# Kernel tuning notes

Measured on AMD Instinct MI355X. Metric: run time of the kernel, lower is better.

The kernel has to match this reference:

```python
import jax, jax.numpy as jnp
import numpy as np

B, T, C, K, NC = 256, 240, 512, 64, 4  # batch, chunk_size, dim, clusters, num_classes+1
EPS = 1e-12


def setup_inputs() -> dict:
    key = jax.random.key(0)
    k1, k2, k3, k4 = jax.random.split(key, 4)
    inputs = jax.random.normal(k1, (B, T, C), dtype=jnp.float32)
    conv_w = jax.random.normal(k2, (K, C), dtype=jnp.float32) * 0.05   # 1x1 assignment conv, no bias (vladv2=False)
    centroids = jax.random.normal(k3, (K, C), dtype=jnp.float32)
    fc_w = jax.random.normal(k4, (NC, K * C), dtype=jnp.float32) * 0.02
    fc_b = jnp.zeros((NC,), dtype=jnp.float32)
    return {"inputs": inputs, "conv_w": conv_w, "centroids": centroids, "fc_w": fc_w, "fc_b": fc_b}


def _l2norm(x, axis):
    return x / jnp.clip(jnp.linalg.norm(x, axis=axis, keepdims=True), EPS)


def reference(inputs, conv_w, centroids, fc_w, fc_b):
    # inputs: [B, T, C]. Torch permutes to NCHW=(B, C, T, 1); feature dim = C.
    x = _l2norm(inputs, axis=-1)                      # normalize_input over feature dim
    # soft assignment: 1x1 conv -> logits [B, T, K], softmax over clusters
    a = jax.nn.softmax(jnp.einsum('btc,kc->btk', x, conv_w), axis=-1)
    # vlad[b,k,c] = sum_t a[b,t,k] * (x[b,t,c] - centroids[k,c])
    #            = einsum(a, x) - (sum_t a) * centroids   (avoids [B,K,C,T] intermediate)
    vlad = jnp.einsum('btk,btc->bkc', a, x) - a.sum(axis=1)[:, :, None] * centroids[None]
    vlad = _l2norm(vlad, axis=-1)                     # intra-normalization over C
    v = vlad.reshape(vlad.shape[0], -1)               # [B, K*C]
    v = _l2norm(v, axis=-1)                           # final L2 normalize
    # dropout is identity in eval mode; fc + sigmoid
    return jax.nn.sigmoid(v @ fc_w.T + fc_b)
```

## Files before the change

kernel.cpp:

```cpp
#include <hip/hip_runtime.h>
#include <hip/hip_bf16.h>
#include <stdint.h>

#define BB 256
#define TT 240
#define CC 512
#define KK 64
#define NCLS 4
#define CHUNK 32
#define NCHUNK 8
#define THREADS 512

typedef __attribute__((ext_vector_type(8))) short bf16x8;
typedef __attribute__((ext_vector_type(4))) float f32x4;

__device__ __forceinline__ unsigned short f2bf(float f) {
    union { float f; unsigned int i; } x; x.f = f;
    unsigned int r = x.i + 0x7FFFu + ((x.i >> 16) & 1u);
    return (unsigned short)(r >> 16);
}
__device__ __forceinline__ unsigned int pk2(float lo, float hi) {
    return ((unsigned int)f2bf(hi) << 16) | (unsigned int)f2bf(lo);
}
__device__ __forceinline__ void LB() {
    asm volatile("s_waitcnt lgkmcnt(0)\n\ts_barrier" ::: "memory");
}

struct alignas(16) SMemChunk {
    unsigned short x[CHUNK][520];
    unsigned short xT[CC][40];
    float logitsA[CHUNK][65];
    unsigned short aT[KK][40];
};
struct alignas(16) SMemEpi { unsigned short vbuf[KK * CC]; };
union SMemU { SMemChunk c; SMemEpi e; };

__global__ __launch_bounds__(THREADS, 2) void netvlad_kernel(
    const float* __restrict__ inp,
    const float* __restrict__ convw,
    const float* __restrict__ cent,
    const float* __restrict__ fcw,
    const float* __restrict__ fcb,
    float* __restrict__ out)
{
    __shared__ SMemU sm;
    __shared__ float sumsq_sh[CHUNK];
    __shared__ float asum[KK];
    __shared__ float ssred[2][KK];
    __shared__ float gred[8];
    __shared__ float fcred[8][NCLS];
    __shared__ float vinv_sh;

    const int tid  = threadIdx.x;
    const int b    = blockIdx.x;
    const int w    = tid >> 6;
    const int lane = tid & 63;
    const int grp  = (lane >> 4) & 3;
    const int col  = lane & 15;
    const int w2   = w >> 1;
    const int half = w & 1;

    if (tid < KK) asum[tid] = 0.f;

    f32x4 acc[16];
    #pragma unroll
    for (int j = 0; j < 16; ++j) acc[j] = (f32x4){0.f, 0.f, 0.f, 0.f};

    bf16x8 cw[16];
    #pragma unroll
    for (int ks = 0; ks < 16; ++ks) {
        const float* p = convw + (size_t)(w2 * 16 + col) * CC + ks * 32 + grp * 8;
        float4 a0 = *(const float4*)p;
        float4 a1 = *(const float4*)(p + 4);
        bf16x8 v;
        v[0] = (short)f2bf(a0.x); v[1] = (short)f2bf(a0.y);
        v[2] = (short)f2bf(a0.z); v[3] = (short)f2bf(a0.w);
        v[4] = (short)f2bf(a1.x); v[5] = (short)f2bf(a1.y);
        v[6] = (short)f2bf(a1.z); v[7] = (short)f2bf(a1.w);
        cw[ks] = v;
    }

    const size_t ibase = (size_t)b * (TT * CC);

    float4 r0[4], r1[4];
    #pragma unroll
    for (int i = 0; i < 4; ++i) {
        int g = tid + i * THREADS;
        int t = g >> 6, c8 = (g & 63) << 3;
        const float* p = inp + ibase + (size_t)t * CC + c8;
        r0[i] = *(const float4*)p;
        r1[i] = *(const float4*)(p + 4);
    }

    for (int ch = 0; ch < NCHUNK; ++ch) {
        const int t0 = ch * CHUNK;
        const int tvalid = (TT - t0 < CHUNK) ? (TT - t0) : CHUNK;

        #pragma unroll
        for (int i = 0; i < 4; ++i) {
            int g = tid + i * THREADS;
            int t = g >> 6, c8 = (g & 63) << 3;
            float4 u0 = r0[i], u1 = r1[i];
            uint4 val = (uint4){pk2(u0.x, u0.y), pk2(u0.z, u0.w),
                                pk2(u1.x, u1.y), pk2(u1.z, u1.w)};
            float s = u0.x*u0.x + u0.y*u0.y + u0.z*u0.z + u0.w*u0.w
                    + u1.x*u1.x + u1.y*u1.y + u1.z*u1.z + u1.w*u1.w;
            if (t >= tvalid) { val = (uint4){0u,0u,0u,0u}; s = 0.f; }
            *(uint4*)&sm.c.x[t][c8] = val;
            s += __shfl_xor(s, 1);  s += __shfl_xor(s, 2);  s += __shfl_xor(s, 4);
            s += __shfl_xor(s, 8);  s += __shfl_xor(s, 16); s += __shfl_xor(s, 32);
            if (lane == 0) sumsq_sh[t] = s;
        }
        if (ch + 1 < NCHUNK) {
            int nt0 = t0 + CHUNK;
            #pragma unroll
            for (int i = 0; i < 4; ++i) {
                int g = tid + i * THREADS;
                int t = g >> 6, c8 = (g & 63) << 3;
                int gt = nt0 + t; if (gt > TT - 1) gt = TT - 1;
                const float* p = inp + ibase + (size_t)gt * CC + c8;
                r0[i] = *(const float4*)p;
                r1[i] = *(const float4*)(p + 4);
            }
        }
        LB();

        {
            int c = tid;
            #pragma unroll
            for (int tb = 0; tb < 4; ++tb) {
                bf16x8 v;
                #pragma unroll
                for (int j = 0; j < 8; ++j) v[j] = (short)sm.c.x[tb * 8 + j][c];
                *(bf16x8*)&sm.c.xT[c][tb * 8] = v;
            }
        }

        {
            f32x4 lt = (f32x4){0.f, 0.f, 0.f, 0.f};
            #pragma unroll
            for (int ks = 0; ks < 16; ++ks) {
                bf16x8 bb = *(const bf16x8*)&sm.c.x[half * 16 + col][ks * 32 + grp * 8];
                lt = __builtin_amdgcn_mfma_f32_16x16x32_bf16(cw[ks], bb, lt, 0, 0, 0);
            }
            #pragma unroll
            for (int r = 0; r < 4; ++r)
                sm.c.logitsA[half * 16 + col][w2 * 16 + grp * 4 + r] = lt[r];
        }
        LB();

        {
            int t = tid >> 4, part = tid & 15;
            float rinv = 1.f / fmaxf(sqrtf(sumsq_sh[t]), 1e-12f);
            rinv = (t < tvalid) ? rinv : 0.f;

            float l[4]; float lmax = -1e30f;
            #pragma unroll
            for (int q = 0; q < 4; ++q) {
                l[q] = sm.c.logitsA[t][q * 16 + part] * rinv;
                lmax = fmaxf(lmax, l[q]);
            }
            lmax = fmaxf(lmax, __shfl_xor(lmax, 1));
            lmax = fmaxf(lmax, __shfl_xor(lmax, 2));
            lmax = fmaxf(lmax, __shfl_xor(lmax, 4));
            lmax = fmaxf(lmax, __shfl_xor(lmax, 8));
            float es = 0.f;
            #pragma unroll
            for (int q = 0; q < 4; ++q) { l[q] = __expf(l[q] - lmax); es += l[q]; }
            es += __shfl_xor(es, 1); es += __shfl_xor(es, 2);
            es += __shfl_xor(es, 4); es += __shfl_xor(es, 8);
            float is = 1.f / es;
            #pragma unroll
            for (int q = 0; q < 4; ++q) {
                float a = l[q] * is;
                sm.c.logitsA[t][q * 16 + part] = a;
                sm.c.aT[q * 16 + part][t] = (unsigned short)f2bf(a * rinv);
            }
        }
        LB();

        if (tid < KK) {
            float s = 0.f;
            for (int t = 0; t < tvalid; ++t) s += sm.c.logitsA[t][tid];
            asum[tid] += s;
        }

        {
            bf16x8 af = *(const bf16x8*)&sm.c.aT[w2 * 16 + col][grp * 8];
            #pragma unroll
            for (int j = 0; j < 16; ++j) {
                bf16x8 bf = *(const bf16x8*)&sm.c.xT[half * 256 + j * 16 + col][grp * 8];
                acc[j] = __builtin_amdgcn_mfma_f32_16x16x32_bf16(af, bf, acc[j], 0, 0, 0);
            }
        }
    }

    LB();

    #pragma unroll
    for (int r = 0; r < 4; ++r) {
        int cl = w2 * 16 + grp * 4 + r;
        float as = asum[cl];
        float ss = 0.f;
        #pragma unroll
        for (int j = 0; j < 16; ++j) {
            int c = half * 256 + j * 16 + col;
            float v = acc[j][r] - as * cent[(size_t)cl * CC + c];
            acc[j][r] = v;
            ss += v * v;
        }
        ss += __shfl_xor(ss, 1); ss += __shfl_xor(ss, 2);
        ss += __shfl_xor(ss, 4); ss += __shfl_xor(ss, 8);
        if (col == 0) ssred[half][cl] = ss;
    }
    LB();

    float contrib = 0.f;
    #pragma unroll
    for (int r = 0; r < 4; ++r) {
        int cl = w2 * 16 + grp * 4 + r;
        float ss = ssred[0][cl] + ssred[1][cl];
        float inv = 1.f / fmaxf(sqrtf(ss), 1e-12f);
        #pragma unroll
        for (int j = 0; j < 16; ++j) {
            float v = acc[j][r] * inv;
            acc[j][r] = v;
            contrib += v * v;
        }
    }
    #pragma unroll
    for (int m = 1; m < 64; m <<= 1) contrib += __shfl_xor(contrib, m);
    if (lane == 0) gred[w] = contrib;
    LB();
    if (tid == 0) {
        float tot = 0.f;
        #pragma unroll
        for (int i = 0; i < 8; ++i) tot += gred[i];
        vinv_sh = 1.f / fmaxf(sqrtf(tot), 1e-12f);
    }
    LB();

    {
        float vinv = vinv_sh;
        #pragma unroll
        for (int r = 0; r < 4; ++r) {
            int cl = w2 * 16 + grp * 4 + r;
            #pragma unroll
            for (int j = 0; j < 16; ++j) {
                int c = half * 256 + j * 16 + col;
                sm.e.vbuf[cl * CC + c] = f2bf(acc[j][r] * vinv);
            }
        }
    }
    LB();

    float pacc[NCLS] = {0.f, 0.f, 0.f, 0.f};
    #pragma unroll
    for (int i = 0; i < 8; ++i) {
        int idx = i * 4096 + tid * 8;
        bf16x8 vv = *(const bf16x8*)&sm.e.vbuf[idx];
        float vf[8];
        #pragma unroll
        for (int h = 0; h < 8; ++h) {
            union { unsigned int u; float f; } cvt;
            cvt.u = ((unsigned int)(unsigned short)vv[h]) << 16;
            vf[h] = cvt.f;
        }
        #pragma unroll
        for (int nc = 0; nc < NCLS; ++nc) {
            const float* wp = fcw + (size_t)nc * (KK * CC) + idx;
            float4 w0 = *(const float4*)wp;
            float4 w1 = *(const float4*)(wp + 4);
            pacc[nc] += vf[0] * w0.x + vf[1] * w0.y + vf[2] * w0.z + vf[3] * w0.w
                      + vf[4] * w1.x + vf[5] * w1.y + vf[6] * w1.z + vf[7] * w1.w;
        }
    }
    #pragma unroll
    for (int nc = 0; nc < NCLS; ++nc) {
        #pragma unroll
        for (int m = 1; m < 64; m <<= 1) pacc[nc] += __shfl_xor(pacc[nc], m);
    }
    if (lane == 0) {
        #pragma unroll
        for (int nc = 0; nc < NCLS; ++nc) fcred[w][nc] = pacc[nc];
    }
    LB();
    if (tid < NCLS) {
        float s = fcb[tid];
        #pragma unroll
        for (int ww = 0; ww < 8; ++ww) s += fcred[ww][tid];
        out[b * NCLS + tid] = 1.f / (1.f + __expf(-s));
    }
}

extern "C" void kernel_launch(void* const* d_in, const int* in_sizes, int n_in,
                              void* d_out, int out_size, void* d_ws, size_t ws_size,
                              hipStream_t stream) {
    const float* inp   = (const float*)d_in[0];
    const float* convw = (const float*)d_in[1];
    const float* cent  = (const float*)d_in[2];
    const float* fcw   = (const float*)d_in[3];
    const float* fcb   = (const float*)d_in[4];
    float* o = (float*)d_out;
    netvlad_kernel<<<BB, THREADS, 0, stream>>>(inp, convw, cent, fcw, fcb, o);
}
```

Measured before the change: 206.2 us.

## Double threads per block to 1024 and split logits GEMM over K halves

```diff
diff --git a/kernel.cpp b/kernel.cpp
--- a/kernel.cpp
+++ b/kernel.cpp
@@ -9,7 +9,7 @@
 #define NCLS 4
 #define CHUNK 32
 #define NCHUNK 8
-#define THREADS 512
+#define THREADS 1024
 
 typedef __attribute__((ext_vector_type(8))) short bf16x8;
 typedef __attribute__((ext_vector_type(4))) float f32x4;
@@ -19,8 +19,10 @@
     unsigned int r = x.i + 0x7FFFu + ((x.i >> 16) & 1u);
     return (unsigned short)(r >> 16);
 }
-__device__ __forceinline__ unsigned int pk2(float lo, float hi) {
-    return ((unsigned int)f2bf(hi) << 16) | (unsigned int)f2bf(lo);
+__device__ __forceinline__ unsigned int pk2cvt(float lo, float hi) {
+    union { __hip_bfloat162 h; unsigned int u; } c;
+    c.h = __float22bfloat162_rn(float2{lo, hi});
+    return c.u;
 }
 __device__ __forceinline__ void LB() {
     asm volatile("s_waitcnt lgkmcnt(0)\n\ts_barrier" ::: "memory");
@@ -29,13 +31,13 @@
 struct alignas(16) SMemChunk {
     unsigned short x[CHUNK][520];
     unsigned short xT[CC][40];
-    float logitsA[CHUNK][65];
+    float logitsP[2][CHUNK][68];
     unsigned short aT[KK][40];
 };
 struct alignas(16) SMemEpi { unsigned short vbuf[KK * CC]; };
 union SMemU { SMemChunk c; SMemEpi e; };
 
-__global__ __launch_bounds__(THREADS, 2) void netvlad_kernel(
+__global__ __launch_bounds__(THREADS, 4) void netvlad_kernel(
     const float* __restrict__ inp,
     const float* __restrict__ convw,
     const float* __restrict__ cent,
@@ -46,9 +48,9 @@
     __shared__ SMemU sm;
     __shared__ float sumsq_sh[CHUNK];
     __shared__ float asum[KK];
-    __shared__ float ssred[2][KK];
-    __shared__ float gred[8];
-    __shared__ float fcred[8][NCLS];
+    __shared__ float ssred[4][KK];
+    __shared__ float gred[16];
+    __shared__ float fcred[16][NCLS];
     __shared__ float vinv_sh;
 
     const int tid  = threadIdx.x;
@@ -57,19 +59,21 @@
     const int lane = tid & 63;
     const int grp  = (lane >> 4) & 3;
     const int col  = lane & 15;
-    const int w2   = w >> 1;
-    const int half = w & 1;
+    const int cg   = w & 3;
+    const int th   = (w >> 2) & 1;
+    const int kh   = w >> 3;
+    const int cq   = w >> 2;
 
     if (tid < KK) asum[tid] = 0.f;
 
-    f32x4 acc[16];
-    #pragma unroll
-    for (int j = 0; j < 16; ++j) acc[j] = (f32x4){0.f, 0.f, 0.f, 0.f};
-
-    bf16x8 cw[16];
-    #pragma unroll
-    for (int ks = 0; ks < 16; ++ks) {
-        const float* p = convw + (size_t)(w2 * 16 + col) * CC + ks * 32 + grp * 8;
+    f32x4 acc[8];
+    #pragma unroll
+    for (int j = 0; j < 8; ++j) acc[j] = (f32x4){0.f, 0.f, 0.f, 0.f};
+
+    bf16x8 cw[8];
+    #pragma unroll
+    for (int s = 0; s < 8; ++s) {
+        const float* p = convw + (size_t)(cg * 16 + col) * CC + (kh * 8 + s) * 32 + grp * 8;
         float4 a0 = *(const float4*)p;
         float4 a1 = *(const float4*)(p + 4);
         bf16x8 v;
@@ -77,14 +81,14 @@
         v[2] = (short)f2bf(a0.z); v[3] = (short)f2bf(a0.w);
         v[4] = (short)f2bf(a1.x); v[5] = (short)f2bf(a1.y);
         v[6] = (short)f2bf(a1.z); v[7] = (short)f2bf(a1.w);
-        cw[ks] = v;
+        cw[s] = v;
     }
 
     const size_t ibase = (size_t)b * (TT * CC);
 
-    float4 r0[4], r1[4];
-    #pragma unroll
-    for (int i = 0; i < 4; ++i) {
+    float4 r0[2], r1[2];
+    #pragma unroll
+    for (int i = 0; i < 2; ++i) {
         int g = tid + i * THREADS;
         int t = g >> 6, c8 = (g & 63) << 3;
         const float* p = inp + ibase + (size_t)t * CC + c8;
@@ -97,12 +101,12 @@
         const int tvalid = (TT - t0 < CHUNK) ? (TT - t0) : CHUNK;
 
         #pragma unroll
-        for (int i = 0; i < 4; ++i) {
+        for (int i = 0; i < 2; ++i) {
             int g = tid + i * THREADS;
             int t = g >> 6, c8 = (g & 63) << 3;
             float4 u0 = r0[i], u1 = r1[i];
-            uint4 val = (uint4){pk2(u0.x, u0.y), pk2(u0.z, u0.w),
-                                pk2(u1.x, u1.y), pk2(u1.z, u1.w)};
+            uint4 val = (uint4){pk2cvt(u0.x, u0.y), pk2cvt(u0.z, u0.w),
+                                pk2cvt(u1.x, u1.y), pk2cvt(u1.z, u1.w)};
             float s = u0.x*u0.x + u0.y*u0.y + u0.z*u0.z + u0.w*u0.w
                     + u1.x*u1.x + u1.y*u1.y + u1.z*u1.z + u1.w*u1.w;
             if (t >= tvalid) { val = (uint4){0u,0u,0u,0u}; s = 0.f; }
@@ -114,7 +118,7 @@
         if (ch + 1 < NCHUNK) {
             int nt0 = t0 + CHUNK;
             #pragma unroll
-            for (int i = 0; i < 4; ++i) {
+            for (int i = 0; i < 2; ++i) {
                 int g = tid + i * THREADS;
                 int t = g >> 6, c8 = (g & 63) << 3;
                 int gt = nt0 + t; if (gt > TT - 1) gt = TT - 1;
@@ -126,30 +130,30 @@
         LB();
 
         {
-            int c = tid;
-            #pragma unroll
-            for (int tb = 0; tb < 4; ++tb) {
+            int c = tid & 511, th2 = tid >> 9;
+            #pragma unroll
+            for (int tb2 = 0; tb2 < 2; ++tb2) {
+                int tb = th2 * 2 + tb2;
                 bf16x8 v;
                 #pragma unroll
                 for (int j = 0; j < 8; ++j) v[j] = (short)sm.c.x[tb * 8 + j][c];
                 *(bf16x8*)&sm.c.xT[c][tb * 8] = v;
             }
         }
-
         {
             f32x4 lt = (f32x4){0.f, 0.f, 0.f, 0.f};
             #pragma unroll
-            for (int ks = 0; ks < 16; ++ks) {
-                bf16x8 bb = *(const bf16x8*)&sm.c.x[half * 16 + col][ks * 32 + grp * 8];
-                lt = __builtin_amdgcn_mfma_f32_16x16x32_bf16(cw[ks], bb, lt, 0, 0, 0);
+            for (int s = 0; s < 8; ++s) {
+                bf16x8 bb = *(const bf16x8*)&sm.c.x[th * 16 + col][(kh * 8 + s) * 32 + grp * 8];
+                lt = __builtin_amdgcn_mfma_f32_16x16x32_bf16(cw[s], bb, lt, 0, 0, 0);
             }
             #pragma unroll
             for (int r = 0; r < 4; ++r)
-                sm.c.logitsA[half * 16 + col][w2 * 16 + grp * 4 + r] = lt[r];
+                sm.c.logitsP[kh][th * 16 + col][cg * 16 + grp * 4 + r] = lt[r];
         }
         LB();
 
-        {
+        if (tid < 512) {
             int t = tid >> 4, part = tid & 15;
             float rinv = 1.f / fmaxf(sqrtf(sumsq_sh[t]), 1e-12f);
             rinv = (t < tvalid) ? rinv : 0.f;
@@ -157,7 +161,8 @@
             float l[4]; float lmax = -1e30f;
             #pragma unroll
             for (int q = 0; q < 4; ++q) {
-                l[q] = sm.c.logitsA[t][q * 16 + part] * rinv;
+                l[q] = (sm.c.logitsP[0][t][q * 16 + part] +
+                        sm.c.logitsP[1][t][q * 16 + part]) * rinv;
                 lmax = fmaxf(lmax, l[q]);
             }
             lmax = fmaxf(lmax, __shfl_xor(lmax, 1));
@@ -173,7 +178,7 @@
             #pragma unroll
             for (int q = 0; q < 4; ++q) {
                 float a = l[q] * is;
-                sm.c.logitsA[t][q * 16 + part] = a;
+                sm.c.logitsP[0][t][q * 16 + part] = a;
                 sm.c.aT[q * 16 + part][t] = (unsigned short)f2bf(a * rinv);
             }
         }
@@ -181,15 +186,14 @@
 
         if (tid < KK) {
             float s = 0.f;
-            for (int t = 0; t < tvalid; ++t) s += sm.c.logitsA[t][tid];
+            for (int t = 0; t < tvalid; ++t) s += sm.c.logitsP[0][t][tid];
             asum[tid] += s;
         }
-
         {
-            bf16x8 af = *(const bf16x8*)&sm.c.aT[w2 * 16 + col][grp * 8];
-            #pragma unroll
-            for (int j = 0; j < 16; ++j) {
-                bf16x8 bf = *(const bf16x8*)&sm.c.xT[half * 256 + j * 16 + col][grp * 8];
+            bf16x8 af = *(const bf16x8*)&sm.c.aT[cg * 16 + col][grp * 8];
+            #pragma unroll
+            for (int j = 0; j < 8; ++j) {
+                bf16x8 bf = *(const bf16x8*)&sm.c.xT[cq * 128 + j * 16 + col][grp * 8];
                 acc[j] = __builtin_amdgcn_mfma_f32_16x16x32_bf16(af, bf, acc[j], 0, 0, 0);
             }
         }
@@ -199,30 +203,30 @@
 
     #pragma unroll
     for (int r = 0; r < 4; ++r) {
-        int cl = w2 * 16 + grp * 4 + r;
+        int cl = cg * 16 + grp * 4 + r;
         float as = asum[cl];
         float ss = 0.f;
         #pragma unroll
-        for (int j = 0; j < 16; ++j) {
-            int c = half * 256 + j * 16 + col;
+        for (int j = 0; j < 8; ++j) {
+            int c = cq * 128 + j * 16 + col;
             float v = acc[j][r] - as * cent[(size_t)cl * CC + c];
             acc[j][r] = v;
             ss += v * v;
         }
         ss += __shfl_xor(ss, 1); ss += __shfl_xor(ss, 2);
         ss += __shfl_xor(ss, 4); ss += __shfl_xor(ss, 8);
-        if (col == 0) ssred[half][cl] = ss;
+        if (col == 0) ssred[cq][cl] = ss;
     }
     LB();
 
     float contrib = 0.f;
     #pragma unroll
     for (int r = 0; r < 4; ++r) {
-        int cl = w2 * 16 + grp * 4 + r;
-        float ss = ssred[0][cl] + ssred[1][cl];
+        int cl = cg * 16 + grp * 4 + r;
+        float ss = ssred[0][cl] + ssred[1][cl] + ssred[2][cl] + ssred[3][cl];
         float inv = 1.f / fmaxf(sqrtf(ss), 1e-12f);
         #pragma unroll
-        for (int j = 0; j < 16; ++j) {
+        for (int j = 0; j < 8; ++j) {
             float v = acc[j][r] * inv;
             acc[j][r] = v;
             contrib += v * v;
@@ -235,7 +239,7 @@
     if (tid == 0) {
         float tot = 0.f;
         #pragma unroll
-        for (int i = 0; i < 8; ++i) tot += gred[i];
+        for (int i = 0; i < 16; ++i) tot += gred[i];
         vinv_sh = 1.f / fmaxf(sqrtf(tot), 1e-12f);
     }
     LB();
@@ -244,10 +248,10 @@
         float vinv = vinv_sh;
         #pragma unroll
         for (int r = 0; r < 4; ++r) {
-            int cl = w2 * 16 + grp * 4 + r;
-            #pragma unroll
-            for (int j = 0; j < 16; ++j) {
-                int c = half * 256 + j * 16 + col;
+            int cl = cg * 16 + grp * 4 + r;
+            #pragma unroll
+            for (int j = 0; j < 8; ++j) {
+                int c = cq * 128 + j * 16 + col;
                 sm.e.vbuf[cl * CC + c] = f2bf(acc[j][r] * vinv);
             }
         }
@@ -256,8 +260,8 @@
 
     float pacc[NCLS] = {0.f, 0.f, 0.f, 0.f};
     #pragma unroll
-    for (int i = 0; i < 8; ++i) {
-        int idx = i * 4096 + tid * 8;
+    for (int i = 0; i < 4; ++i) {
+        int idx = i * 8192 + tid * 8;
         bf16x8 vv = *(const bf16x8*)&sm.e.vbuf[idx];
         float vf[8];
         #pragma unroll
@@ -288,7 +292,7 @@
     if (tid < NCLS) {
         float s = fcb[tid];
         #pragma unroll
-        for (int ww = 0; ww < 8; ++ww) s += fcred[ww][tid];
+        for (int ww = 0; ww < 16; ++ww) s += fcred[ww][tid];
         out[b * NCLS + tid] = 1.f / (1.f + __expf(-s));
     }
 }
```

New measurement: 205.7 us. Within noise of the previous version (-0.3%).
